# Kernel optimization log

Measured on AMD Instinct MI355X. Metric: run time of the kernel, lower is better.

Reference implementation:

```python
import jax, jax.numpy as jnp
import numpy as np

H_DIM = 1024
N_NODES = 50000


def setup_inputs() -> dict:
    key = jax.random.key(0)
    ks = jax.random.split(key, 8)
    a = 1.0 / np.sqrt(H_DIM).astype(np.float32)  # torch Linear default U(-1/sqrt(fan_in), 1/sqrt(fan_in))
    # scale activations by 0.1 so the double exp (exp of scores, then softmax) stays finite in fp32
    H = jax.random.normal(ks[0], (N_NODES, H_DIM), jnp.float32) * 0.1
    h_t = jax.random.normal(ks[1], (1, H_DIM), jnp.float32) * 0.1
    W0 = jax.random.uniform(ks[2], (H_DIM, H_DIM), jnp.float32, -a, a)
    b0 = jax.random.uniform(ks[3], (H_DIM,), jnp.float32, -a, a)
    W1 = jax.random.uniform(ks[4], (H_DIM, H_DIM), jnp.float32, -a, a)
    b1 = jax.random.uniform(ks[5], (H_DIM,), jnp.float32, -a, a)
    W2 = jax.random.uniform(ks[6], (H_DIM, H_DIM), jnp.float32, -a, a)
    b2 = jax.random.uniform(ks[7], (H_DIM,), jnp.float32, -a, a)
    return {"H": H, "h_t": h_t, "W0": W0, "b0": b0, "W1": W1, "b1": b1, "W2": W2, "b2": b2}


def reference(H, h_t, W0, b0, W1, b1, W2, b2):
    # query vector w_0(h_t): [1, h_dim]
    q = h_t @ W0.T + b0
    # per-node raw score node.h @ w_0(h_t).T, then exp (as in the original loop): [N]
    scores = jnp.exp((H @ q.T).squeeze(-1))
    # original applies softmax on top of the exp'd scores (double exp) -- faithful
    w = jax.nn.softmax(scores)
    # weighted sum of node states: [1, h_dim]
    e_s = (w @ H)[None, :]
    # tanh-gated projection
    return jnp.tanh(e_s @ W1.T + b1 + h_t @ W2.T + b2)
```

## Files before the change

kernel.cpp:

```cpp
#include <hip/hip_runtime.h>
#include <hip/hip_bf16.h>

#define D 1024

typedef unsigned int u32;
typedef __attribute__((ext_vector_type(4))) unsigned int u32x4;

__device__ __forceinline__ float bflo(u32 u) { return __uint_as_float(u << 16); }
__device__ __forceinline__ float bfhi(u32 u) { return __uint_as_float(u & 0xffff0000u); }
__device__ __forceinline__ float bf1(const void* p, int j) {
    unsigned short s = ((const unsigned short*)p)[j];
    return __uint_as_float(((u32)s) << 16);
}

__device__ __forceinline__ float waveReduceSum(float v) {
#pragma unroll
    for (int off = 32; off > 0; off >>= 1) v += __shfl_xor(v, off, 64);
    return v;
}

__global__ __launch_bounds__(64) void k_probe(const u32* __restrict__ htw,
                                              int* __restrict__ flag) {
    int lane = threadIdx.x;
    u32 w = htw[lane];
    u32 e = (w >> 7) & 0xFF;
    float c = (e >= 100 && e <= 126) ? 1.f : 0.f;
    c = waveReduceSum(c);
    if (lane == 0) *flag = (c >= 56.f) ? 1 : 0;
}

__global__ __launch_bounds__(256) void k_q(const int* __restrict__ flag,
                                           const void* __restrict__ W0,
                                           const void* __restrict__ ht,
                                           const void* __restrict__ b0,
                                           float* __restrict__ q) {
    int wid = threadIdx.x >> 6, lane = threadIdx.x & 63;
    int j = blockIdx.x * 4 + wid;
    int isBf16 = *flag;
    float s = 0.f;
    if (isBf16) {
        const u32x4* wrow = (const u32x4*)((const __hip_bfloat16*)W0 + (size_t)j * D);
        const u32x4* hv = (const u32x4*)ht;
#pragma unroll
        for (int half = 0; half < 2; ++half) {
            u32x4 a = wrow[half * 64 + lane];
            u32x4 b = hv[half * 64 + lane];
#pragma unroll
            for (int t = 0; t < 4; ++t) {
                s += bflo(a[t]) * bflo(b[t]);
                s += bfhi(a[t]) * bfhi(b[t]);
            }
        }
    } else {
        const float4* wrow = (const float4*)((const float*)W0 + (size_t)j * D);
        const float4* hv = (const float4*)ht;
#pragma unroll
        for (int t = 0; t < 4; ++t) {
            float4 a = wrow[t * 64 + lane];
            float4 b = hv[t * 64 + lane];
            s += a.x * b.x + a.y * b.y + a.z * b.z + a.w * b.w;
        }
    }
    s = waveReduceSum(s);
    if (lane == 0) {
        float bias = isBf16 ? bf1(b0, j) : ((const float*)b0)[j];
        q[j] = s + bias;
    }
}

__device__ __forceinline__ void loadRow(const void* __restrict__ Hm, int r,
                                        int isBf16, int lane, float* h) {
    if (isBf16) {
        const u32x4* hr = (const u32x4*)((const __hip_bfloat16*)Hm + (size_t)r * D);
        u32x4 a = hr[lane];
        u32x4 b = hr[64 + lane];
#pragma unroll
        for (int t = 0; t < 4; ++t) {
            h[2 * t] = bflo(a[t]);     h[2 * t + 1] = bfhi(a[t]);
            h[8 + 2 * t] = bflo(b[t]); h[8 + 2 * t + 1] = bfhi(b[t]);
        }
    } else {
        const float4* hr = (const float4*)((const float*)Hm + (size_t)r * D);
#pragma unroll
        for (int t = 0; t < 4; ++t) {
            float4 a = hr[t * 64 + lane];
            h[t * 4 + 0] = a.x; h[t * 4 + 1] = a.y;
            h[t * 4 + 2] = a.z; h[t * 4 + 3] = a.w;
        }
    }
}

__device__ __forceinline__ float dotTree(const float* h, const float* qr) {
    float p[16];
#pragma unroll
    for (int j = 0; j < 16; ++j) p[j] = h[j] * qr[j];
#pragma unroll
    for (int step = 1; step < 16; step <<= 1)
#pragma unroll
        for (int j = 0; j < 16; j += 2 * step) p[j] += p[j + step];
    return p[0];
}

__global__ __launch_bounds__(512) void k_pass(const int* __restrict__ flag,
                                              const void* __restrict__ Hm,
                                              const float* __restrict__ q,
                                              float* __restrict__ accp,
                                              float* __restrict__ lvals,
                                              int N, int totalWaves) {
    __shared__ float lacc[8][D];
    __shared__ float ll[8];
    int wid = threadIdx.x >> 6, lane = threadIdx.x & 63;
    int gw = blockIdx.x * 8 + wid;
    int isBf16 = *flag;

    int col[16];
    if (isBf16) {
#pragma unroll
        for (int j = 0; j < 8; ++j) { col[j] = lane * 8 + j; col[8 + j] = 512 + lane * 8 + j; }
    } else {
#pragma unroll
        for (int t = 0; t < 4; ++t)
#pragma unroll
            for (int u = 0; u < 4; ++u) col[t * 4 + u] = t * 256 + lane * 4 + u;
    }
    float qr[16];
#pragma unroll
    for (int j = 0; j < 16; ++j) qr[j] = q[col[j]];

    float l = 0.f;
    float acc[16];
#pragma unroll
    for (int j = 0; j < 16; ++j) acc[j] = 0.f;

    int r = gw;
    for (; r + totalWaves < N; r += 2 * totalWaves) {
        float h0[16], h1[16];
        loadRow(Hm, r, isBf16, lane, h0);
        loadRow(Hm, r + totalWaves, isBf16, lane, h1);
        float d0 = dotTree(h0, qr);
        float d1 = dotTree(h1, qr);
        d0 = waveReduceSum(d0);
        d1 = waveReduceSum(d1);
        float p0 = __expf(__expf(d0));
        float p1 = __expf(__expf(d1));
        l += p0 + p1;
#pragma unroll
        for (int j = 0; j < 16; ++j) acc[j] += p0 * h0[j] + p1 * h1[j];
    }
    if (r < N) {
        float h0[16];
        loadRow(Hm, r, isBf16, lane, h0);
        float d0 = waveReduceSum(dotTree(h0, qr));
        float p0 = __expf(__expf(d0));
        l += p0;
#pragma unroll
        for (int j = 0; j < 16; ++j) acc[j] += p0 * h0[j];
    }

#pragma unroll
    for (int j = 0; j < 16; ++j) lacc[wid][col[j]] = acc[j];
    if (lane == 0) ll[wid] = l;
    __syncthreads();
    float* dst = accp + (size_t)blockIdx.x * D;
    for (int k = threadIdx.x; k < D; k += 512) {
        float s = 0.f;
#pragma unroll
        for (int w = 0; w < 8; ++w) s += lacc[w][k];
        dst[k] = s;
    }
    if (threadIdx.x == 0) {
        float s = 0.f;
#pragma unroll
        for (int w = 0; w < 8; ++w) s += ll[w];
        lvals[blockIdx.x] = s;
    }
}

__global__ __launch_bounds__(256) void k_fin(const float* __restrict__ accp,
                                             const float* __restrict__ lvals,
                                             float* __restrict__ e_s,
                                             float* __restrict__ Ls, int B) {
    __shared__ float part[4][64];
    int t = threadIdx.x, lane = t & 63, chunk = t >> 6;
    int col = blockIdx.x * 64 + lane;
    int rpc = B >> 2;
    float s = 0.f;
    for (int b = chunk * rpc; b < (chunk + 1) * rpc; ++b)
        s += accp[(size_t)b * D + col];
    part[chunk][lane] = s;
    __syncthreads();
    if (t < 64) e_s[col] = part[0][lane] + part[1][lane] + part[2][lane] + part[3][lane];
    if (blockIdx.x == 0 && chunk == 3) {
        float ls = 0.f;
        for (int b = lane; b < B; b += 64) ls += lvals[b];
        ls = waveReduceSum(ls);
        if (lane == 0) *Ls = ls;
    }
}

__global__ __launch_bounds__(256) void k_out(const int* __restrict__ flag,
                                             const void* __restrict__ W1,
                                             const void* __restrict__ b1,
                                             const void* __restrict__ W2,
                                             const void* __restrict__ b2,
                                             const void* __restrict__ ht,
                                             const float* __restrict__ e_s,
                                             const float* __restrict__ Ls,
                                             void* __restrict__ out) {
    int wid = threadIdx.x >> 6, lane = threadIdx.x & 63;
    int j = blockIdx.x * 4 + wid;
    int isBf16 = *flag;
    float s1 = 0.f, s2 = 0.f;
    if (isBf16) {
        const u32x4* w1r = (const u32x4*)((const __hip_bfloat16*)W1 + (size_t)j * D);
        const u32x4* w2r = (const u32x4*)((const __hip_bfloat16*)W2 + (size_t)j * D);
        const u32x4* hv = (const u32x4*)ht;
        int c0 = lane * 8;
#pragma unroll
        for (int half = 0; half < 2; ++half) {
            u32x4 a = w1r[half * 64 + lane];
            u32x4 b = w2r[half * 64 + lane];
            u32x4 hh = hv[half * 64 + lane];
            const float4* ev = (const float4*)(e_s + half * 512 + c0);
            float4 ea = ev[0], eb = ev[1];
            float e[8] = {ea.x, ea.y, ea.z, ea.w, eb.x, eb.y, eb.z, eb.w};
#pragma unroll
            for (int t = 0; t < 4; ++t) {
                s1 += bflo(a[t]) * e[2 * t] + bfhi(a[t]) * e[2 * t + 1];
                s2 += bflo(b[t]) * bflo(hh[t]) + bfhi(b[t]) * bfhi(hh[t]);
            }
        }
    } else {
        const float4* w1r = (const float4*)((const float*)W1 + (size_t)j * D);
        const float4* w2r = (const float4*)((const float*)W2 + (size_t)j * D);
        const float4* hv = (const float4*)ht;
        const float4* ev = (const float4*)e_s;
#pragma unroll
        for (int t = 0; t < 4; ++t) {
            float4 a = w1r[t * 64 + lane];
            float4 b = w2r[t * 64 + lane];
            float4 hh = hv[t * 64 + lane];
            float4 ee = ev[t * 64 + lane];
            s1 += a.x * ee.x + a.y * ee.y + a.z * ee.z + a.w * ee.w;
            s2 += b.x * hh.x + b.y * hh.y + b.z * hh.z + b.w * hh.w;
        }
    }
    s1 = waveReduceSum(s1);
    s2 = waveReduceSum(s2);
    if (lane == 0) {
        float bias1 = isBf16 ? bf1(b1, j) : ((const float*)b1)[j];
        float bias2 = isBf16 ? bf1(b2, j) : ((const float*)b2)[j];
        float r = tanhf(s1 / (*Ls) + bias1 + s2 + bias2);
        if (isBf16) ((__hip_bfloat16*)out)[j] = __float2bfloat16(r);
        else        ((float*)out)[j] = r;
    }
}

extern "C" void kernel_launch(void* const* d_in, const int* in_sizes, int n_in,
                              void* d_out, int out_size, void* d_ws, size_t ws_size,
                              hipStream_t stream) {
    const void* H  = d_in[0];
    const void* ht = d_in[1];
    const void* W0 = d_in[2];
    const void* b0 = d_in[3];
    const void* W1 = d_in[4];
    const void* b1 = d_in[5];
    const void* W2 = d_in[6];
    const void* b2 = d_in[7];
    int N = in_sizes[0] / D;

    float* wsf  = (float*)d_ws;
    int*   flag = (int*)wsf;
    float* Ls   = wsf + 1;
    float* q    = wsf + 64;
    float* e_s  = wsf + 1088;
    float* lvals= wsf + 2112;
    float* accp = wsf + 4096;

    int B = 512;
    while (B > 64 && ws_size < (size_t)(4096 + (size_t)B * D) * 4) B >>= 1;

    k_probe<<<1, 64, 0, stream>>>((const u32*)ht, flag);
    k_q<<<256, 256, 0, stream>>>(flag, W0, ht, b0, q);
    k_pass<<<B, 512, 0, stream>>>(flag, H, q, accp, lvals, N, B * 8);
    k_fin<<<D / 64, 256, 0, stream>>>(accp, lvals, e_s, Ls, B);
    k_out<<<256, 256, 0, stream>>>(flag, W1, b1, W2, b2, ht, e_s, Ls, d_out);
}
```

Baseline: 336.2 us.

## Fuse all stages into one cooperative kernel with grid syncs

Replaces the five separate launches (probe, q projection, main pass, final reduction, output projection) with a single cooperative kernel of 256 blocks that uses grid-wide syncs between stages. Each block recomputes the dtype probe locally, and the final column reduction now uses wave shuffles over 256 partials per block. The aim is to remove launch overhead and inter-kernel gaps. In exchange, the main pass uses a fixed 256 blocks instead of up to 512, which may lower memory-level parallelism, and the grid syncs add their own cost.

```diff
diff --git a/kernel.cpp b/kernel.cpp
--- a/kernel.cpp
+++ b/kernel.cpp
@@ -1,7 +1,12 @@
 #include <hip/hip_runtime.h>
 #include <hip/hip_bf16.h>
+#include <hip/hip_cooperative_groups.h>
+
+namespace cg = cooperative_groups;
 
 #define D 1024
+#define NB 256
+#define TPB 512
 
 typedef unsigned int u32;
 typedef __attribute__((ext_vector_type(4))) unsigned int u32x4;
@@ -17,55 +22,6 @@
 #pragma unroll
     for (int off = 32; off > 0; off >>= 1) v += __shfl_xor(v, off, 64);
     return v;
-}
-
-__global__ __launch_bounds__(64) void k_probe(const u32* __restrict__ htw,
-                                              int* __restrict__ flag) {
-    int lane = threadIdx.x;
-    u32 w = htw[lane];
-    u32 e = (w >> 7) & 0xFF;
-    float c = (e >= 100 && e <= 126) ? 1.f : 0.f;
-    c = waveReduceSum(c);
-    if (lane == 0) *flag = (c >= 56.f) ? 1 : 0;
-}
-
-__global__ __launch_bounds__(256) void k_q(const int* __restrict__ flag,
-                                           const void* __restrict__ W0,
-                                           const void* __restrict__ ht,
-                                           const void* __restrict__ b0,
-                                           float* __restrict__ q) {
-    int wid = threadIdx.x >> 6, lane = threadIdx.x & 63;
-    int j = blockIdx.x * 4 + wid;
-    int isBf16 = *flag;
-    float s = 0.f;
-    if (isBf16) {
-        const u32x4* wrow = (const u32x4*)((const __hip_bfloat16*)W0 + (size_t)j * D);
-        const u32x4* hv = (const u32x4*)ht;
-#pragma unroll
-        for (int half = 0; half < 2; ++half) {
-            u32x4 a = wrow[half * 64 + lane];
-            u32x4 b = hv[half * 64 + lane];
-#pragma unroll
-            for (int t = 0; t < 4; ++t) {
-                s += bflo(a[t]) * bflo(b[t]);
-                s += bfhi(a[t]) * bfhi(b[t]);
-            }
-        }
-    } else {
-        const float4* wrow = (const float4*)((const float*)W0 + (size_t)j * D);
-        const float4* hv = (const float4*)ht;
-#pragma unroll
-        for (int t = 0; t < 4; ++t) {
-            float4 a = wrow[t * 64 + lane];
-            float4 b = hv[t * 64 + lane];
-            s += a.x * b.x + a.y * b.y + a.z * b.z + a.w * b.w;
-        }
-    }
-    s = waveReduceSum(s);
-    if (lane == 0) {
-        float bias = isBf16 ? bf1(b0, j) : ((const float*)b0)[j];
-        q[j] = s + bias;
-    }
 }
 
 __device__ __forceinline__ void loadRow(const void* __restrict__ Hm, int r,
@@ -101,158 +57,204 @@
     return p[0];
 }
 
-__global__ __launch_bounds__(512) void k_pass(const int* __restrict__ flag,
-                                              const void* __restrict__ Hm,
-                                              const float* __restrict__ q,
-                                              float* __restrict__ accp,
-                                              float* __restrict__ lvals,
-                                              int N, int totalWaves) {
+__global__ __launch_bounds__(TPB) void k_all(
+    const void* __restrict__ Hm, const void* __restrict__ ht,
+    const void* __restrict__ W0, const void* __restrict__ b0,
+    const void* __restrict__ W1, const void* __restrict__ b1,
+    const void* __restrict__ W2, const void* __restrict__ b2,
+    void* __restrict__ out,
+    float* __restrict__ q, float* __restrict__ accp,
+    float* __restrict__ lvals, float* __restrict__ e_s,
+    float* __restrict__ Ls, int N) {
+    cg::grid_group grid = cg::this_grid();
     __shared__ float lacc[8][D];
     __shared__ float ll[8];
+    __shared__ float4 redf[4];
     int wid = threadIdx.x >> 6, lane = threadIdx.x & 63;
-    int gw = blockIdx.x * 8 + wid;
-    int isBf16 = *flag;
-
-    int col[16];
-    if (isBf16) {
-#pragma unroll
-        for (int j = 0; j < 8; ++j) { col[j] = lane * 8 + j; col[8 + j] = 512 + lane * 8 + j; }
-    } else {
-#pragma unroll
-        for (int t = 0; t < 4; ++t)
-#pragma unroll
-            for (int u = 0; u < 4; ++u) col[t * 4 + u] = t * 256 + lane * 4 + u;
-    }
-    float qr[16];
-#pragma unroll
-    for (int j = 0; j < 16; ++j) qr[j] = q[col[j]];
-
-    float l = 0.f;
-    float acc[16];
-#pragma unroll
-    for (int j = 0; j < 16; ++j) acc[j] = 0.f;
-
-    int r = gw;
-    for (; r + totalWaves < N; r += 2 * totalWaves) {
-        float h0[16], h1[16];
-        loadRow(Hm, r, isBf16, lane, h0);
-        loadRow(Hm, r + totalWaves, isBf16, lane, h1);
-        float d0 = dotTree(h0, qr);
-        float d1 = dotTree(h1, qr);
-        d0 = waveReduceSum(d0);
-        d1 = waveReduceSum(d1);
-        float p0 = __expf(__expf(d0));
-        float p1 = __expf(__expf(d1));
-        l += p0 + p1;
-#pragma unroll
-        for (int j = 0; j < 16; ++j) acc[j] += p0 * h0[j] + p1 * h1[j];
-    }
-    if (r < N) {
-        float h0[16];
-        loadRow(Hm, r, isBf16, lane, h0);
-        float d0 = waveReduceSum(dotTree(h0, qr));
-        float p0 = __expf(__expf(d0));
-        l += p0;
-#pragma unroll
-        for (int j = 0; j < 16; ++j) acc[j] += p0 * h0[j];
-    }
-
-#pragma unroll
-    for (int j = 0; j < 16; ++j) lacc[wid][col[j]] = acc[j];
-    if (lane == 0) ll[wid] = l;
-    __syncthreads();
-    float* dst = accp + (size_t)blockIdx.x * D;
-    for (int k = threadIdx.x; k < D; k += 512) {
+
+    int isBf16;
+    {
+        u32 w = ((const u32*)ht)[lane];
+        u32 e = (w >> 7) & 0xFF;
+        float c = (e >= 100 && e <= 126) ? 1.f : 0.f;
+        c = waveReduceSum(c);
+        isBf16 = (c >= 56.f) ? 1 : 0;
+    }
+
+    if (wid < 4) {
+        int j = blockIdx.x * 4 + wid;
         float s = 0.f;
-#pragma unroll
-        for (int w = 0; w < 8; ++w) s += lacc[w][k];
-        dst[k] = s;
-    }
-    if (threadIdx.x == 0) {
-        float s = 0.f;
-#pragma unroll
-        for (int w = 0; w < 8; ++w) s += ll[w];
-        lvals[blockIdx.x] = s;
-    }
-}
-
-__global__ __launch_bounds__(256) void k_fin(const float* __restrict__ accp,
-                                             const float* __restrict__ lvals,
-                                             float* __restrict__ e_s,
-                                             float* __restrict__ Ls, int B) {
-    __shared__ float part[4][64];
-    int t = threadIdx.x, lane = t & 63, chunk = t >> 6;
-    int col = blockIdx.x * 64 + lane;
-    int rpc = B >> 2;
-    float s = 0.f;
-    for (int b = chunk * rpc; b < (chunk + 1) * rpc; ++b)
-        s += accp[(size_t)b * D + col];
-    part[chunk][lane] = s;
-    __syncthreads();
-    if (t < 64) e_s[col] = part[0][lane] + part[1][lane] + part[2][lane] + part[3][lane];
-    if (blockIdx.x == 0 && chunk == 3) {
-        float ls = 0.f;
-        for (int b = lane; b < B; b += 64) ls += lvals[b];
-        ls = waveReduceSum(ls);
-        if (lane == 0) *Ls = ls;
-    }
-}
-
-__global__ __launch_bounds__(256) void k_out(const int* __restrict__ flag,
-                                             const void* __restrict__ W1,
-                                             const void* __restrict__ b1,
-                                             const void* __restrict__ W2,
-                                             const void* __restrict__ b2,
-                                             const void* __restrict__ ht,
-                                             const float* __restrict__ e_s,
-                                             const float* __restrict__ Ls,
-                                             void* __restrict__ out) {
-    int wid = threadIdx.x >> 6, lane = threadIdx.x & 63;
-    int j = blockIdx.x * 4 + wid;
-    int isBf16 = *flag;
-    float s1 = 0.f, s2 = 0.f;
-    if (isBf16) {
-        const u32x4* w1r = (const u32x4*)((const __hip_bfloat16*)W1 + (size_t)j * D);
-        const u32x4* w2r = (const u32x4*)((const __hip_bfloat16*)W2 + (size_t)j * D);
-        const u32x4* hv = (const u32x4*)ht;
-        int c0 = lane * 8;
-#pragma unroll
-        for (int half = 0; half < 2; ++half) {
-            u32x4 a = w1r[half * 64 + lane];
-            u32x4 b = w2r[half * 64 + lane];
-            u32x4 hh = hv[half * 64 + lane];
-            const float4* ev = (const float4*)(e_s + half * 512 + c0);
-            float4 ea = ev[0], eb = ev[1];
-            float e[8] = {ea.x, ea.y, ea.z, ea.w, eb.x, eb.y, eb.z, eb.w};
+        if (isBf16) {
+            const u32x4* wrow = (const u32x4*)((const __hip_bfloat16*)W0 + (size_t)j * D);
+            const u32x4* hv = (const u32x4*)ht;
+#pragma unroll
+            for (int half = 0; half < 2; ++half) {
+                u32x4 a = wrow[half * 64 + lane];
+                u32x4 b = hv[half * 64 + lane];
+#pragma unroll
+                for (int t = 0; t < 4; ++t) {
+                    s += bflo(a[t]) * bflo(b[t]);
+                    s += bfhi(a[t]) * bfhi(b[t]);
+                }
+            }
+        } else {
+            const float4* wrow = (const float4*)((const float*)W0 + (size_t)j * D);
+            const float4* hv = (const float4*)ht;
 #pragma unroll
             for (int t = 0; t < 4; ++t) {
-                s1 += bflo(a[t]) * e[2 * t] + bfhi(a[t]) * e[2 * t + 1];
-                s2 += bflo(b[t]) * bflo(hh[t]) + bfhi(b[t]) * bfhi(hh[t]);
-            }
-        }
-    } else {
-        const float4* w1r = (const float4*)((const float*)W1 + (size_t)j * D);
-        const float4* w2r = (const float4*)((const float*)W2 + (size_t)j * D);
-        const float4* hv = (const float4*)ht;
-        const float4* ev = (const float4*)e_s;
-#pragma unroll
-        for (int t = 0; t < 4; ++t) {
-            float4 a = w1r[t * 64 + lane];
-            float4 b = w2r[t * 64 + lane];
-            float4 hh = hv[t * 64 + lane];
-            float4 ee = ev[t * 64 + lane];
-            s1 += a.x * ee.x + a.y * ee.y + a.z * ee.z + a.w * ee.w;
-            s2 += b.x * hh.x + b.y * hh.y + b.z * hh.z + b.w * hh.w;
-        }
-    }
-    s1 = waveReduceSum(s1);
-    s2 = waveReduceSum(s2);
-    if (lane == 0) {
-        float bias1 = isBf16 ? bf1(b1, j) : ((const float*)b1)[j];
-        float bias2 = isBf16 ? bf1(b2, j) : ((const float*)b2)[j];
-        float r = tanhf(s1 / (*Ls) + bias1 + s2 + bias2);
-        if (isBf16) ((__hip_bfloat16*)out)[j] = __float2bfloat16(r);
-        else        ((float*)out)[j] = r;
+                float4 a = wrow[t * 64 + lane];
+                float4 b = hv[t * 64 + lane];
+                s += a.x * b.x + a.y * b.y + a.z * b.z + a.w * b.w;
+            }
+        }
+        s = waveReduceSum(s);
+        if (lane == 0) {
+            float bias = isBf16 ? bf1(b0, j) : ((const float*)b0)[j];
+            q[j] = s + bias;
+        }
+    }
+    grid.sync();
+
+    {
+        int col[16];
+        if (isBf16) {
+#pragma unroll
+            for (int j = 0; j < 8; ++j) { col[j] = lane * 8 + j; col[8 + j] = 512 + lane * 8 + j; }
+        } else {
+#pragma unroll
+            for (int t = 0; t < 4; ++t)
+#pragma unroll
+                for (int u = 0; u < 4; ++u) col[t * 4 + u] = t * 256 + lane * 4 + u;
+        }
+        float qr[16];
+#pragma unroll
+        for (int j = 0; j < 16; ++j) qr[j] = q[col[j]];
+
+        float l = 0.f;
+        float acc[16];
+#pragma unroll
+        for (int j = 0; j < 16; ++j) acc[j] = 0.f;
+
+        const int totalWaves = NB * 8;
+        int gw = blockIdx.x * 8 + wid;
+        int r = gw;
+        for (; r + totalWaves < N; r += 2 * totalWaves) {
+            float h0[16], h1[16];
+            loadRow(Hm, r, isBf16, lane, h0);
+            loadRow(Hm, r + totalWaves, isBf16, lane, h1);
+            float d0 = dotTree(h0, qr);
+            float d1 = dotTree(h1, qr);
+            d0 = waveReduceSum(d0);
+            d1 = waveReduceSum(d1);
+            float p0 = __expf(__expf(d0));
+            float p1 = __expf(__expf(d1));
+            l += p0 + p1;
+#pragma unroll
+            for (int j = 0; j < 16; ++j) acc[j] += p0 * h0[j] + p1 * h1[j];
+        }
+        if (r < N) {
+            float h0[16];
+            loadRow(Hm, r, isBf16, lane, h0);
+            float d0 = waveReduceSum(dotTree(h0, qr));
+            float p0 = __expf(__expf(d0));
+            l += p0;
+#pragma unroll
+            for (int j = 0; j < 16; ++j) acc[j] += p0 * h0[j];
+        }
+
+#pragma unroll
+        for (int j = 0; j < 16; ++j) lacc[wid][col[j]] = acc[j];
+        if (lane == 0) ll[wid] = l;
+        __syncthreads();
+        float* dst = accp + (size_t)blockIdx.x * D;
+        for (int k = threadIdx.x; k < D; k += TPB) {
+            float s = 0.f;
+#pragma unroll
+            for (int w = 0; w < 8; ++w) s += lacc[w][k];
+            dst[k] = s;
+        }
+        if (threadIdx.x == 0) {
+            float s = 0.f;
+#pragma unroll
+            for (int w = 0; w < 8; ++w) s += ll[w];
+            lvals[blockIdx.x] = s;
+        }
+    }
+    grid.sync();
+
+    {
+        if (threadIdx.x < 256) {
+            float4 v = *(const float4*)(accp + (size_t)threadIdx.x * D + blockIdx.x * 4);
+            v.x = waveReduceSum(v.x);
+            v.y = waveReduceSum(v.y);
+            v.z = waveReduceSum(v.z);
+            v.w = waveReduceSum(v.w);
+            if (lane == 0) redf[wid] = v;
+        }
+        if (blockIdx.x == 0 && wid == 4) {
+            float ls = lvals[lane] + lvals[lane + 64] + lvals[lane + 128] + lvals[lane + 192];
+            ls = waveReduceSum(ls);
+            if (lane == 0) *Ls = ls;
+        }
+        __syncthreads();
+        if (threadIdx.x == 0) {
+            float4 a = redf[0], b = redf[1], c = redf[2], d = redf[3];
+            float4 r;
+            r.x = a.x + b.x + c.x + d.x;
+            r.y = a.y + b.y + c.y + d.y;
+            r.z = a.z + b.z + c.z + d.z;
+            r.w = a.w + b.w + c.w + d.w;
+            *(float4*)(e_s + blockIdx.x * 4) = r;
+        }
+    }
+    grid.sync();
+
+    if (wid < 4) {
+        int j = blockIdx.x * 4 + wid;
+        float s1 = 0.f, s2 = 0.f;
+        if (isBf16) {
+            const u32x4* w1r = (const u32x4*)((const __hip_bfloat16*)W1 + (size_t)j * D);
+            const u32x4* w2r = (const u32x4*)((const __hip_bfloat16*)W2 + (size_t)j * D);
+            const u32x4* hv = (const u32x4*)ht;
+            int c0 = lane * 8;
+#pragma unroll
+            for (int half = 0; half < 2; ++half) {
+                u32x4 a = w1r[half * 64 + lane];
+                u32x4 b = w2r[half * 64 + lane];
+                u32x4 hh = hv[half * 64 + lane];
+                const float4* ev = (const float4*)(e_s + half * 512 + c0);
+                float4 ea = ev[0], eb = ev[1];
+                float e[8] = {ea.x, ea.y, ea.z, ea.w, eb.x, eb.y, eb.z, eb.w};
+#pragma unroll
+                for (int t = 0; t < 4; ++t) {
+                    s1 += bflo(a[t]) * e[2 * t] + bfhi(a[t]) * e[2 * t + 1];
+                    s2 += bflo(b[t]) * bflo(hh[t]) + bfhi(b[t]) * bfhi(hh[t]);
+                }
+            }
+        } else {
+            const float4* w1r = (const float4*)((const float*)W1 + (size_t)j * D);
+            const float4* w2r = (const float4*)((const float*)W2 + (size_t)j * D);
+            const float4* hv = (const float4*)ht;
+            const float4* ev = (const float4*)e_s;
+#pragma unroll
+            for (int t = 0; t < 4; ++t) {
+                float4 a = w1r[t * 64 + lane];
+                float4 b = w2r[t * 64 + lane];
+                float4 hh = hv[t * 64 + lane];
+                float4 ee = ev[t * 64 + lane];
+                s1 += a.x * ee.x + a.y * ee.y + a.z * ee.z + a.w * ee.w;
+                s2 += b.x * hh.x + b.y * hh.y + b.z * hh.z + b.w * hh.w;
+            }
+        }
+        s1 = waveReduceSum(s1);
+        s2 = waveReduceSum(s2);
+        if (lane == 0) {
+            float bias1 = isBf16 ? bf1(b1, j) : ((const float*)b1)[j];
+            float bias2 = isBf16 ? bf1(b2, j) : ((const float*)b2)[j];
+            float r = tanhf(s1 / (*Ls) + bias1 + s2 + bias2);
+            if (isBf16) ((__hip_bfloat16*)out)[j] = __float2bfloat16(r);
+            else        ((float*)out)[j] = r;
+        }
     }
 }
 
@@ -267,22 +269,20 @@
     const void* b1 = d_in[5];
     const void* W2 = d_in[6];
     const void* b2 = d_in[7];
+    void* out = d_out;
     int N = in_sizes[0] / D;
 
-    float* wsf  = (float*)d_ws;
-    int*   flag = (int*)wsf;
-    float* Ls   = wsf + 1;
-    float* q    = wsf + 64;
-    float* e_s  = wsf + 1088;
-    float* lvals= wsf + 2112;
-    float* accp = wsf + 4096;
-
-    int B = 512;
-    while (B > 64 && ws_size < (size_t)(4096 + (size_t)B * D) * 4) B >>= 1;
-
-    k_probe<<<1, 64, 0, stream>>>((const u32*)ht, flag);
-    k_q<<<256, 256, 0, stream>>>(flag, W0, ht, b0, q);
-    k_pass<<<B, 512, 0, stream>>>(flag, H, q, accp, lvals, N, B * 8);
-    k_fin<<<D / 64, 256, 0, stream>>>(accp, lvals, e_s, Ls, B);
-    k_out<<<256, 256, 0, stream>>>(flag, W1, b1, W2, b2, ht, e_s, Ls, d_out);
-}
+    float* wsf   = (float*)d_ws;
+    float* q     = wsf;
+    float* e_s   = wsf + 1024;
+    float* Ls    = wsf + 2048;
+    float* lvals = wsf + 2112;
+    float* accp  = wsf + 4096;
+
+    void* args[] = {(void*)&H, (void*)&ht, (void*)&W0, (void*)&b0,
+                    (void*)&W1, (void*)&b1, (void*)&W2, (void*)&b2,
+                    (void*)&out, (void*)&q, (void*)&accp, (void*)&lvals,
+                    (void*)&e_s, (void*)&Ls, (void*)&N};
+    hipLaunchCooperativeKernel((const void*)k_all, dim3(NB), dim3(TPB),
+                               args, 0, stream);
+}
```

Measured after the change: 392.8 us. 16.9% more time.

## Split fused score/weighted-sum pass into separate score and column-sum kernels

Applied to the files above, without the earlier changes.

Replaces the single fused pass (per-wave dot product, double exp, and row accumulation) with two kernels. The first computes 16 rows of scores per wave, keeps 8 row loads in flight, batches the shuffle reductions, and writes per-row weights plus block partial sums. The second streams H by columns, each block covering a contiguous row range, and accumulates the weighted sum. This aims for more memory-level parallelism and less per-row reduction latency, at the cost of reading H twice and an extra workspace buffer whose size is no longer checked against ws_size.

```diff
diff --git a/kernel.cpp b/kernel.cpp
--- a/kernel.cpp
+++ b/kernel.cpp
@@ -5,6 +5,7 @@
 
 typedef unsigned int u32;
 typedef __attribute__((ext_vector_type(4))) unsigned int u32x4;
+typedef __attribute__((ext_vector_type(4))) unsigned short u16x4;
 
 __device__ __forceinline__ float bflo(u32 u) { return __uint_as_float(u << 16); }
 __device__ __forceinline__ float bfhi(u32 u) { return __uint_as_float(u & 0xffff0000u); }
@@ -68,118 +69,151 @@
     }
 }
 
-__device__ __forceinline__ void loadRow(const void* __restrict__ Hm, int r,
-                                        int isBf16, int lane, float* h) {
+__global__ __launch_bounds__(256) void k_score(const int* __restrict__ flag,
+                                               const void* __restrict__ Hm,
+                                               const float* __restrict__ q,
+                                               float* __restrict__ w,
+                                               float* __restrict__ lvals,
+                                               int N) {
+    __shared__ float ls[4];
+    int wid = threadIdx.x >> 6, lane = threadIdx.x & 63;
+    int gw = blockIdx.x * 4 + wid;
+    int isBf16 = *flag;
+
+    float qr[16];
     if (isBf16) {
-        const u32x4* hr = (const u32x4*)((const __hip_bfloat16*)Hm + (size_t)r * D);
-        u32x4 a = hr[lane];
-        u32x4 b = hr[64 + lane];
-#pragma unroll
-        for (int t = 0; t < 4; ++t) {
-            h[2 * t] = bflo(a[t]);     h[2 * t + 1] = bfhi(a[t]);
-            h[8 + 2 * t] = bflo(b[t]); h[8 + 2 * t + 1] = bfhi(b[t]);
+#pragma unroll
+        for (int j = 0; j < 8; ++j) {
+            qr[j] = q[lane * 8 + j];
+            qr[8 + j] = q[512 + lane * 8 + j];
         }
     } else {
-        const float4* hr = (const float4*)((const float*)Hm + (size_t)r * D);
-#pragma unroll
-        for (int t = 0; t < 4; ++t) {
-            float4 a = hr[t * 64 + lane];
-            h[t * 4 + 0] = a.x; h[t * 4 + 1] = a.y;
-            h[t * 4 + 2] = a.z; h[t * 4 + 3] = a.w;
-        }
-    }
-}
-
-__device__ __forceinline__ float dotTree(const float* h, const float* qr) {
-    float p[16];
-#pragma unroll
-    for (int j = 0; j < 16; ++j) p[j] = h[j] * qr[j];
-#pragma unroll
-    for (int step = 1; step < 16; step <<= 1)
-#pragma unroll
-        for (int j = 0; j < 16; j += 2 * step) p[j] += p[j + step];
-    return p[0];
-}
-
-__global__ __launch_bounds__(512) void k_pass(const int* __restrict__ flag,
+#pragma unroll
+        for (int t = 0; t < 4; ++t)
+#pragma unroll
+            for (int u = 0; u < 4; ++u) qr[t * 4 + u] = q[t * 256 + lane * 4 + u];
+    }
+
+    float lsum = 0.f;
+#pragma unroll
+    for (int half = 0; half < 2; ++half) {
+        int r0 = gw * 16 + half * 8;
+        float d[8];
+#pragma unroll
+        for (int i = 0; i < 8; ++i) {
+            int r = r0 + i;
+            float dd = 0.f;
+            if (r < N) {
+                if (isBf16) {
+                    const u32x4* hr = (const u32x4*)((const __hip_bfloat16*)Hm + (size_t)r * D);
+                    u32x4 a = hr[lane];
+                    u32x4 b = hr[64 + lane];
+#pragma unroll
+                    for (int t = 0; t < 4; ++t) {
+                        dd += bflo(a[t]) * qr[2 * t] + bfhi(a[t]) * qr[2 * t + 1];
+                        dd += bflo(b[t]) * qr[8 + 2 * t] + bfhi(b[t]) * qr[8 + 2 * t + 1];
+                    }
+                } else {
+                    const float4* hr = (const float4*)((const float*)Hm + (size_t)r * D);
+#pragma unroll
+                    for (int t = 0; t < 4; ++t) {
+                        float4 a = hr[t * 64 + lane];
+                        dd += a.x * qr[t * 4] + a.y * qr[t * 4 + 1] +
+                              a.z * qr[t * 4 + 2] + a.w * qr[t * 4 + 3];
+                    }
+                }
+            }
+            d[i] = dd;
+        }
+#pragma unroll
+        for (int off = 32; off > 0; off >>= 1) {
+#pragma unroll
+            for (int i = 0; i < 8; ++i) d[i] += __shfl_xor(d[i], off, 64);
+        }
+        float p[8];
+#pragma unroll
+        for (int i = 0; i < 8; ++i) p[i] = __expf(__expf(d[i]));
+        if (r0 + 8 <= N) {
+            if (lane == 0) {
+                float4 w0 = {p[0], p[1], p[2], p[3]};
+                float4 w1 = {p[4], p[5], p[6], p[7]};
+                *(float4*)(w + r0) = w0;
+                *(float4*)(w + r0 + 4) = w1;
+            }
+#pragma unroll
+            for (int i = 0; i < 8; ++i) lsum += p[i];
+        } else {
+#pragma unroll
+            for (int i = 0; i < 8; ++i) {
+                if (r0 + i < N) {
+                    if (lane == 0) w[r0 + i] = p[i];
+                    lsum += p[i];
+                }
+            }
+        }
+    }
+    if (lane == 0) ls[wid] = lsum;
+    __syncthreads();
+    if (threadIdx.x == 0) lvals[blockIdx.x] = ls[0] + ls[1] + ls[2] + ls[3];
+}
+
+__global__ __launch_bounds__(256) void k_wsum(const int* __restrict__ flag,
                                               const void* __restrict__ Hm,
-                                              const float* __restrict__ q,
+                                              const float* __restrict__ w,
                                               float* __restrict__ accp,
-                                              float* __restrict__ lvals,
-                                              int N, int totalWaves) {
-    __shared__ float lacc[8][D];
-    __shared__ float ll[8];
-    int wid = threadIdx.x >> 6, lane = threadIdx.x & 63;
-    int gw = blockIdx.x * 8 + wid;
+                                              int N, int rpb) {
     int isBf16 = *flag;
-
-    int col[16];
+    int c = threadIdx.x * 4;
+    int rb = blockIdx.x * rpb;
+    int re = min(N, rb + rpb);
+    float a0 = 0.f, a1 = 0.f, a2 = 0.f, a3 = 0.f;
+    int r = rb;
     if (isBf16) {
-#pragma unroll
-        for (int j = 0; j < 8; ++j) { col[j] = lane * 8 + j; col[8 + j] = 512 + lane * 8 + j; }
+        const unsigned short* Hb = (const unsigned short*)Hm;
+        for (; r + 8 <= re; r += 8) {
+#pragma unroll
+            for (int i = 0; i < 8; ++i) {
+                float wr = w[r + i];
+                u16x4 hv = *(const u16x4*)(Hb + (size_t)(r + i) * D + c);
+                a0 += wr * __uint_as_float(((u32)hv[0]) << 16);
+                a1 += wr * __uint_as_float(((u32)hv[1]) << 16);
+                a2 += wr * __uint_as_float(((u32)hv[2]) << 16);
+                a3 += wr * __uint_as_float(((u32)hv[3]) << 16);
+            }
+        }
+        for (; r < re; ++r) {
+            float wr = w[r];
+            u16x4 hv = *(const u16x4*)(Hb + (size_t)r * D + c);
+            a0 += wr * __uint_as_float(((u32)hv[0]) << 16);
+            a1 += wr * __uint_as_float(((u32)hv[1]) << 16);
+            a2 += wr * __uint_as_float(((u32)hv[2]) << 16);
+            a3 += wr * __uint_as_float(((u32)hv[3]) << 16);
+        }
     } else {
-#pragma unroll
-        for (int t = 0; t < 4; ++t)
-#pragma unroll
-            for (int u = 0; u < 4; ++u) col[t * 4 + u] = t * 256 + lane * 4 + u;
-    }
-    float qr[16];
-#pragma unroll
-    for (int j = 0; j < 16; ++j) qr[j] = q[col[j]];
-
-    float l = 0.f;
-    float acc[16];
-#pragma unroll
-    for (int j = 0; j < 16; ++j) acc[j] = 0.f;
-
-    int r = gw;
-    for (; r + totalWaves < N; r += 2 * totalWaves) {
-        float h0[16], h1[16];
-        loadRow(Hm, r, isBf16, lane, h0);
-        loadRow(Hm, r + totalWaves, isBf16, lane, h1);
-        float d0 = dotTree(h0, qr);
-        float d1 = dotTree(h1, qr);
-        d0 = waveReduceSum(d0);
-        d1 = waveReduceSum(d1);
-        float p0 = __expf(__expf(d0));
-        float p1 = __expf(__expf(d1));
-        l += p0 + p1;
-#pragma unroll
-        for (int j = 0; j < 16; ++j) acc[j] += p0 * h0[j] + p1 * h1[j];
-    }
-    if (r < N) {
-        float h0[16];
-        loadRow(Hm, r, isBf16, lane, h0);
-        float d0 = waveReduceSum(dotTree(h0, qr));
-        float p0 = __expf(__expf(d0));
-        l += p0;
-#pragma unroll
-        for (int j = 0; j < 16; ++j) acc[j] += p0 * h0[j];
-    }
-
-#pragma unroll
-    for (int j = 0; j < 16; ++j) lacc[wid][col[j]] = acc[j];
-    if (lane == 0) ll[wid] = l;
-    __syncthreads();
-    float* dst = accp + (size_t)blockIdx.x * D;
-    for (int k = threadIdx.x; k < D; k += 512) {
-        float s = 0.f;
-#pragma unroll
-        for (int w = 0; w < 8; ++w) s += lacc[w][k];
-        dst[k] = s;
-    }
-    if (threadIdx.x == 0) {
-        float s = 0.f;
-#pragma unroll
-        for (int w = 0; w < 8; ++w) s += ll[w];
-        lvals[blockIdx.x] = s;
-    }
+        const float* Hf = (const float*)Hm;
+        for (; r + 8 <= re; r += 8) {
+#pragma unroll
+            for (int i = 0; i < 8; ++i) {
+                float wr = w[r + i];
+                float4 hv = *(const float4*)(Hf + (size_t)(r + i) * D + c);
+                a0 += wr * hv.x; a1 += wr * hv.y; a2 += wr * hv.z; a3 += wr * hv.w;
+            }
+        }
+        for (; r < re; ++r) {
+            float wr = w[r];
+            float4 hv = *(const float4*)(Hf + (size_t)r * D + c);
+            a0 += wr * hv.x; a1 += wr * hv.y; a2 += wr * hv.z; a3 += wr * hv.w;
+        }
+    }
+    float4 res = {a0, a1, a2, a3};
+    *(float4*)(accp + (size_t)blockIdx.x * D + c) = res;
 }
 
 __global__ __launch_bounds__(256) void k_fin(const float* __restrict__ accp,
                                              const float* __restrict__ lvals,
                                              float* __restrict__ e_s,
-                                             float* __restrict__ Ls, int B) {
+                                             float* __restrict__ Ls,
+                                             int B, int NL) {
     __shared__ float part[4][64];
     int t = threadIdx.x, lane = t & 63, chunk = t >> 6;
     int col = blockIdx.x * 64 + lane;
@@ -192,7 +226,7 @@
     if (t < 64) e_s[col] = part[0][lane] + part[1][lane] + part[2][lane] + part[3][lane];
     if (blockIdx.x == 0 && chunk == 3) {
         float ls = 0.f;
-        for (int b = lane; b < B; b += 64) ls += lvals[b];
+        for (int b = lane; b < NL; b += 64) ls += lvals[b];
         ls = waveReduceSum(ls);
         if (lane == 0) *Ls = ls;
     }
@@ -269,20 +303,23 @@
     const void* b2 = d_in[7];
     int N = in_sizes[0] / D;
 
-    float* wsf  = (float*)d_ws;
-    int*   flag = (int*)wsf;
-    float* Ls   = wsf + 1;
-    float* q    = wsf + 64;
-    float* e_s  = wsf + 1088;
-    float* lvals= wsf + 2112;
-    float* accp = wsf + 4096;
-
-    int B = 512;
-    while (B > 64 && ws_size < (size_t)(4096 + (size_t)B * D) * 4) B >>= 1;
+    const int WSB = 512;
+    int rpb = (N + WSB - 1) / WSB;
+    int nsc = (N + 63) / 64;
+
+    float* wsf   = (float*)d_ws;
+    int*   flag  = (int*)wsf;
+    float* Ls    = wsf + 1;
+    float* q     = wsf + 64;
+    float* e_s   = wsf + 1088;
+    float* lvals = wsf + 2112;
+    float* w     = wsf + 3136;
+    float* accp  = wsf + 3136 + ((N + 63) & ~63);
 
     k_probe<<<1, 64, 0, stream>>>((const u32*)ht, flag);
     k_q<<<256, 256, 0, stream>>>(flag, W0, ht, b0, q);
-    k_pass<<<B, 512, 0, stream>>>(flag, H, q, accp, lvals, N, B * 8);
-    k_fin<<<D / 64, 256, 0, stream>>>(accp, lvals, e_s, Ls, B);
+    k_score<<<nsc, 256, 0, stream>>>(flag, H, q, w, lvals, N);
+    k_wsum<<<WSB, 256, 0, stream>>>(flag, H, w, accp, N, rpb);
+    k_fin<<<D / 64, 256, 0, stream>>>(accp, lvals, e_s, Ls, WSB, nsc);
     k_out<<<256, 256, 0, stream>>>(flag, W1, b1, W2, b2, ht, e_s, Ls, d_out);
 }
```

Result: slower. 370.6 us (+10.2%).

## Fuse probe and final reduction into neighboring kernels, precompute W2 projection early

Applied to the files above, without the earlier changes.

Removes the separate probe and final-reduction launches. Each kernel now recomputes the bf16 probe inline, and the last block of the pass kernel, found with an atomic counter, does the cross-block reduction. The h_t@W2 term plus both biases moves into the query kernel so the output kernel reads only W1. The dot product in the main loop switches from a tree sum to a linear sum with interleaved shuffles. This trades launch overhead and some output-kernel traffic for a serialized tail in one block and a fixed grid size that no longer checks workspace size.

```diff
diff --git a/kernel.cpp b/kernel.cpp
--- a/kernel.cpp
+++ b/kernel.cpp
@@ -19,27 +19,19 @@
     return v;
 }
 
-__global__ __launch_bounds__(64) void k_probe(const u32* __restrict__ htw,
-                                              int* __restrict__ flag) {
-    int lane = threadIdx.x;
-    u32 w = htw[lane];
+__device__ __forceinline__ int probeBf16(const void* ht, int lane) {
+    u32 w = ((const u32*)ht)[lane];
     u32 e = (w >> 7) & 0xFF;
     float c = (e >= 100 && e <= 126) ? 1.f : 0.f;
     c = waveReduceSum(c);
-    if (lane == 0) *flag = (c >= 56.f) ? 1 : 0;
-}
-
-__global__ __launch_bounds__(256) void k_q(const int* __restrict__ flag,
-                                           const void* __restrict__ W0,
-                                           const void* __restrict__ ht,
-                                           const void* __restrict__ b0,
-                                           float* __restrict__ q) {
-    int wid = threadIdx.x >> 6, lane = threadIdx.x & 63;
-    int j = blockIdx.x * 4 + wid;
-    int isBf16 = *flag;
+    return (c >= 56.f) ? 1 : 0;
+}
+
+__device__ __forceinline__ float rowDotHt(const void* W, const void* ht,
+                                          int j, int lane, int isBf16) {
     float s = 0.f;
     if (isBf16) {
-        const u32x4* wrow = (const u32x4*)((const __hip_bfloat16*)W0 + (size_t)j * D);
+        const u32x4* wrow = (const u32x4*)((const __hip_bfloat16*)W + (size_t)j * D);
         const u32x4* hv = (const u32x4*)ht;
 #pragma unroll
         for (int half = 0; half < 2; ++half) {
@@ -52,7 +44,7 @@
             }
         }
     } else {
-        const float4* wrow = (const float4*)((const float*)W0 + (size_t)j * D);
+        const float4* wrow = (const float4*)((const float*)W + (size_t)j * D);
         const float4* hv = (const float4*)ht;
 #pragma unroll
         for (int t = 0; t < 4; ++t) {
@@ -61,57 +53,53 @@
             s += a.x * b.x + a.y * b.y + a.z * b.z + a.w * b.w;
         }
     }
-    s = waveReduceSum(s);
-    if (lane == 0) {
-        float bias = isBf16 ? bf1(b0, j) : ((const float*)b0)[j];
-        q[j] = s + bias;
-    }
-}
-
-__device__ __forceinline__ void loadRow(const void* __restrict__ Hm, int r,
-                                        int isBf16, int lane, float* h) {
-    if (isBf16) {
-        const u32x4* hr = (const u32x4*)((const __hip_bfloat16*)Hm + (size_t)r * D);
-        u32x4 a = hr[lane];
-        u32x4 b = hr[64 + lane];
-#pragma unroll
-        for (int t = 0; t < 4; ++t) {
-            h[2 * t] = bflo(a[t]);     h[2 * t + 1] = bfhi(a[t]);
-            h[8 + 2 * t] = bflo(b[t]); h[8 + 2 * t + 1] = bfhi(b[t]);
+    return waveReduceSum(s);
+}
+
+__global__ __launch_bounds__(512) void k_q(const void* __restrict__ W0,
+                                           const void* __restrict__ b0,
+                                           const void* __restrict__ W2,
+                                           const void* __restrict__ b1,
+                                           const void* __restrict__ b2,
+                                           const void* __restrict__ ht,
+                                           float* __restrict__ q,
+                                           float* __restrict__ t2,
+                                           int* __restrict__ counter) {
+    int wid = threadIdx.x >> 6, lane = threadIdx.x & 63;
+    int isBf16 = probeBf16(ht, lane);
+    if (blockIdx.x == 0 && threadIdx.x == 0) *counter = 0;
+    int j = blockIdx.x * 4 + (wid & 3);
+    if (wid < 4) {
+        float s = rowDotHt(W0, ht, j, lane, isBf16);
+        if (lane == 0) {
+            float bias = isBf16 ? bf1(b0, j) : ((const float*)b0)[j];
+            q[j] = s + bias;
         }
     } else {
-        const float4* hr = (const float4*)((const float*)Hm + (size_t)r * D);
-#pragma unroll
-        for (int t = 0; t < 4; ++t) {
-            float4 a = hr[t * 64 + lane];
-            h[t * 4 + 0] = a.x; h[t * 4 + 1] = a.y;
-            h[t * 4 + 2] = a.z; h[t * 4 + 3] = a.w;
-        }
-    }
-}
-
-__device__ __forceinline__ float dotTree(const float* h, const float* qr) {
-    float p[16];
-#pragma unroll
-    for (int j = 0; j < 16; ++j) p[j] = h[j] * qr[j];
-#pragma unroll
-    for (int step = 1; step < 16; step <<= 1)
-#pragma unroll
-        for (int j = 0; j < 16; j += 2 * step) p[j] += p[j + step];
-    return p[0];
-}
-
-__global__ __launch_bounds__(512) void k_pass(const int* __restrict__ flag,
-                                              const void* __restrict__ Hm,
-                                              const float* __restrict__ q,
-                                              float* __restrict__ accp,
-                                              float* __restrict__ lvals,
-                                              int N, int totalWaves) {
+        float s = rowDotHt(W2, ht, j, lane, isBf16);
+        if (lane == 0) {
+            float bb = isBf16 ? (bf1(b1, j) + bf1(b2, j))
+                              : (((const float*)b1)[j] + ((const float*)b2)[j]);
+            t2[j] = s + bb;
+        }
+    }
+}
+
+#define PB 512
+__global__ __launch_bounds__(512, 4) void k_pass(const void* __restrict__ Hm,
+                                                 const void* __restrict__ ht,
+                                                 const float* __restrict__ q,
+                                                 float* __restrict__ accp,
+                                                 float* __restrict__ lvals,
+                                                 float* __restrict__ e_s,
+                                                 float* __restrict__ Ls,
+                                                 int* __restrict__ counter,
+                                                 int N) {
     __shared__ float lacc[8][D];
     __shared__ float ll[8];
+    __shared__ int isLast;
     int wid = threadIdx.x >> 6, lane = threadIdx.x & 63;
-    int gw = blockIdx.x * 8 + wid;
-    int isBf16 = *flag;
+    int isBf16 = probeBf16(ht, lane);
 
     int col[16];
     if (isBf16) {
@@ -132,15 +120,42 @@
 #pragma unroll
     for (int j = 0; j < 16; ++j) acc[j] = 0.f;
 
+    const int totalWaves = PB * 8;
+    int gw = blockIdx.x * 8 + wid;
     int r = gw;
     for (; r + totalWaves < N; r += 2 * totalWaves) {
         float h0[16], h1[16];
-        loadRow(Hm, r, isBf16, lane, h0);
-        loadRow(Hm, r + totalWaves, isBf16, lane, h1);
-        float d0 = dotTree(h0, qr);
-        float d1 = dotTree(h1, qr);
-        d0 = waveReduceSum(d0);
-        d1 = waveReduceSum(d1);
+        if (isBf16) {
+            const u32x4* hr0 = (const u32x4*)((const __hip_bfloat16*)Hm + (size_t)r * D);
+            const u32x4* hr1 = (const u32x4*)((const __hip_bfloat16*)Hm + (size_t)(r + totalWaves) * D);
+            u32x4 a0 = hr0[lane], b0v = hr0[64 + lane];
+            u32x4 a1 = hr1[lane], b1v = hr1[64 + lane];
+#pragma unroll
+            for (int t = 0; t < 4; ++t) {
+                h0[2 * t] = bflo(a0[t]);     h0[2 * t + 1] = bfhi(a0[t]);
+                h0[8 + 2 * t] = bflo(b0v[t]); h0[8 + 2 * t + 1] = bfhi(b0v[t]);
+                h1[2 * t] = bflo(a1[t]);     h1[2 * t + 1] = bfhi(a1[t]);
+                h1[8 + 2 * t] = bflo(b1v[t]); h1[8 + 2 * t + 1] = bfhi(b1v[t]);
+            }
+        } else {
+            const float4* hr0 = (const float4*)((const float*)Hm + (size_t)r * D);
+            const float4* hr1 = (const float4*)((const float*)Hm + (size_t)(r + totalWaves) * D);
+#pragma unroll
+            for (int t = 0; t < 4; ++t) {
+                float4 a = hr0[t * 64 + lane];
+                float4 b = hr1[t * 64 + lane];
+                h0[t * 4] = a.x; h0[t * 4 + 1] = a.y; h0[t * 4 + 2] = a.z; h0[t * 4 + 3] = a.w;
+                h1[t * 4] = b.x; h1[t * 4 + 1] = b.y; h1[t * 4 + 2] = b.z; h1[t * 4 + 3] = b.w;
+            }
+        }
+        float d0 = 0.f, d1 = 0.f;
+#pragma unroll
+        for (int j = 0; j < 16; ++j) { d0 += h0[j] * qr[j]; d1 += h1[j] * qr[j]; }
+#pragma unroll
+        for (int off = 32; off > 0; off >>= 1) {
+            d0 += __shfl_xor(d0, off, 64);
+            d1 += __shfl_xor(d1, off, 64);
+        }
         float p0 = __expf(__expf(d0));
         float p1 = __expf(__expf(d1));
         l += p0 + p1;
@@ -149,8 +164,26 @@
     }
     if (r < N) {
         float h0[16];
-        loadRow(Hm, r, isBf16, lane, h0);
-        float d0 = waveReduceSum(dotTree(h0, qr));
+        if (isBf16) {
+            const u32x4* hr0 = (const u32x4*)((const __hip_bfloat16*)Hm + (size_t)r * D);
+            u32x4 a0 = hr0[lane], b0v = hr0[64 + lane];
+#pragma unroll
+            for (int t = 0; t < 4; ++t) {
+                h0[2 * t] = bflo(a0[t]);     h0[2 * t + 1] = bfhi(a0[t]);
+                h0[8 + 2 * t] = bflo(b0v[t]); h0[8 + 2 * t + 1] = bfhi(b0v[t]);
+            }
+        } else {
+            const float4* hr0 = (const float4*)((const float*)Hm + (size_t)r * D);
+#pragma unroll
+            for (int t = 0; t < 4; ++t) {
+                float4 a = hr0[t * 64 + lane];
+                h0[t * 4] = a.x; h0[t * 4 + 1] = a.y; h0[t * 4 + 2] = a.z; h0[t * 4 + 3] = a.w;
+            }
+        }
+        float d0 = 0.f;
+#pragma unroll
+        for (int j = 0; j < 16; ++j) d0 += h0[j] * qr[j];
+        d0 = waveReduceSum(d0);
         float p0 = __expf(__expf(d0));
         l += p0;
 #pragma unroll
@@ -174,83 +207,69 @@
         for (int w = 0; w < 8; ++w) s += ll[w];
         lvals[blockIdx.x] = s;
     }
-}
-
-__global__ __launch_bounds__(256) void k_fin(const float* __restrict__ accp,
-                                             const float* __restrict__ lvals,
-                                             float* __restrict__ e_s,
-                                             float* __restrict__ Ls, int B) {
-    __shared__ float part[4][64];
-    int t = threadIdx.x, lane = t & 63, chunk = t >> 6;
-    int col = blockIdx.x * 64 + lane;
-    int rpc = B >> 2;
-    float s = 0.f;
-    for (int b = chunk * rpc; b < (chunk + 1) * rpc; ++b)
-        s += accp[(size_t)b * D + col];
-    part[chunk][lane] = s;
+
+    __threadfence();
+    if (threadIdx.x == 0) {
+        int t = atomicAdd(counter, 1);
+        isLast = (t == (int)gridDim.x - 1);
+    }
     __syncthreads();
-    if (t < 64) e_s[col] = part[0][lane] + part[1][lane] + part[2][lane] + part[3][lane];
-    if (blockIdx.x == 0 && chunk == 3) {
-        float ls = 0.f;
-        for (int b = lane; b < B; b += 64) ls += lvals[b];
-        ls = waveReduceSum(ls);
-        if (lane == 0) *Ls = ls;
-    }
-}
-
-__global__ __launch_bounds__(256) void k_out(const int* __restrict__ flag,
-                                             const void* __restrict__ W1,
-                                             const void* __restrict__ b1,
-                                             const void* __restrict__ W2,
-                                             const void* __restrict__ b2,
+    if (!isLast) return;
+    __threadfence();
+    {
+        int c = (threadIdx.x & 255) * 4;
+        if (threadIdx.x < 256) {
+            float4 s = {0.f, 0.f, 0.f, 0.f};
+            for (int b = 0; b < PB; ++b) {
+                float4 v = *(const float4*)(accp + (size_t)b * D + c);
+                s.x += v.x; s.y += v.y; s.z += v.z; s.w += v.w;
+            }
+            *(float4*)(e_s + c) = s;
+        } else if (threadIdx.x >= 256 && threadIdx.x < 320) {
+            float ls = 0.f;
+            for (int b = lane; b < PB; b += 64) ls += lvals[b];
+            ls = waveReduceSum(ls);
+            if (lane == 0) *Ls = ls;
+        }
+    }
+}
+
+__global__ __launch_bounds__(256) void k_out(const void* __restrict__ W1,
                                              const void* __restrict__ ht,
                                              const float* __restrict__ e_s,
+                                             const float* __restrict__ t2,
                                              const float* __restrict__ Ls,
                                              void* __restrict__ out) {
     int wid = threadIdx.x >> 6, lane = threadIdx.x & 63;
     int j = blockIdx.x * 4 + wid;
-    int isBf16 = *flag;
-    float s1 = 0.f, s2 = 0.f;
+    int isBf16 = probeBf16(ht, lane);
+    float s1 = 0.f;
     if (isBf16) {
         const u32x4* w1r = (const u32x4*)((const __hip_bfloat16*)W1 + (size_t)j * D);
-        const u32x4* w2r = (const u32x4*)((const __hip_bfloat16*)W2 + (size_t)j * D);
-        const u32x4* hv = (const u32x4*)ht;
         int c0 = lane * 8;
 #pragma unroll
         for (int half = 0; half < 2; ++half) {
             u32x4 a = w1r[half * 64 + lane];
-            u32x4 b = w2r[half * 64 + lane];
-            u32x4 hh = hv[half * 64 + lane];
             const float4* ev = (const float4*)(e_s + half * 512 + c0);
             float4 ea = ev[0], eb = ev[1];
             float e[8] = {ea.x, ea.y, ea.z, ea.w, eb.x, eb.y, eb.z, eb.w};
 #pragma unroll
-            for (int t = 0; t < 4; ++t) {
+            for (int t = 0; t < 4; ++t)
                 s1 += bflo(a[t]) * e[2 * t] + bfhi(a[t]) * e[2 * t + 1];
-                s2 += bflo(b[t]) * bflo(hh[t]) + bfhi(b[t]) * bfhi(hh[t]);
-            }
         }
     } else {
         const float4* w1r = (const float4*)((const float*)W1 + (size_t)j * D);
-        const float4* w2r = (const float4*)((const float*)W2 + (size_t)j * D);
-        const float4* hv = (const float4*)ht;
         const float4* ev = (const float4*)e_s;
 #pragma unroll
         for (int t = 0; t < 4; ++t) {
             float4 a = w1r[t * 64 + lane];
-            float4 b = w2r[t * 64 + lane];
-            float4 hh = hv[t * 64 + lane];
             float4 ee = ev[t * 64 + lane];
             s1 += a.x * ee.x + a.y * ee.y + a.z * ee.z + a.w * ee.w;
-            s2 += b.x * hh.x + b.y * hh.y + b.z * hh.z + b.w * hh.w;
         }
     }
     s1 = waveReduceSum(s1);
-    s2 = waveReduceSum(s2);
     if (lane == 0) {
-        float bias1 = isBf16 ? bf1(b1, j) : ((const float*)b1)[j];
-        float bias2 = isBf16 ? bf1(b2, j) : ((const float*)b2)[j];
-        float r = tanhf(s1 / (*Ls) + bias1 + s2 + bias2);
+        float r = tanhf(s1 / (*Ls) + t2[j]);
         if (isBf16) ((__hip_bfloat16*)out)[j] = __float2bfloat16(r);
         else        ((float*)out)[j] = r;
     }
@@ -269,20 +288,16 @@
     const void* b2 = d_in[7];
     int N = in_sizes[0] / D;
 
-    float* wsf  = (float*)d_ws;
-    int*   flag = (int*)wsf;
-    float* Ls   = wsf + 1;
-    float* q    = wsf + 64;
-    float* e_s  = wsf + 1088;
-    float* lvals= wsf + 2112;
-    float* accp = wsf + 4096;
-
-    int B = 512;
-    while (B > 64 && ws_size < (size_t)(4096 + (size_t)B * D) * 4) B >>= 1;
-
-    k_probe<<<1, 64, 0, stream>>>((const u32*)ht, flag);
-    k_q<<<256, 256, 0, stream>>>(flag, W0, ht, b0, q);
-    k_pass<<<B, 512, 0, stream>>>(flag, H, q, accp, lvals, N, B * 8);
-    k_fin<<<D / 64, 256, 0, stream>>>(accp, lvals, e_s, Ls, B);
-    k_out<<<256, 256, 0, stream>>>(flag, W1, b1, W2, b2, ht, e_s, Ls, d_out);
-}
+    float* wsf    = (float*)d_ws;
+    int*   counter= (int*)wsf;
+    float* Ls     = wsf + 1;
+    float* q      = wsf + 64;
+    float* t2     = wsf + 1088;
+    float* e_s    = wsf + 2112;
+    float* lvals  = wsf + 3136;
+    float* accp   = wsf + 4160;
+
+    k_q<<<256, 512, 0, stream>>>(W0, b0, W2, b1, b2, ht, q, t2, counter);
+    k_pass<<<PB, 512, 0, stream>>>(H, ht, q, accp, lvals, e_s, Ls, counter, N);
+    k_out<<<256, 256, 0, stream>>>(W1, ht, e_s, t2, Ls, d_out);
+}
```

Measured after the change: 483.2 us. 43.7% more time.
